# Performance work log

Measured on AMD Instinct MI355X. Metric: run time of the kernel, lower is better.

## Reference

```python
import jax, jax.numpy as jnp
import numpy as np
from jax import lax

CONF_THRESH = 0.5   # from module __init__
NMS_THRESH = 0.4    # from module __init__
TOP_K = 1000        # static pre-NMS candidate cap (JAX needs fixed shapes)

B, N, C = 16, 22743, 80  # batch, predictions (608px, 3 scales), COCO classes


def setup_inputs() -> dict:
    key = jax.random.key(0)
    # YOLOv3 raw output: [B, N, 5+C] = (cx, cy, w, h, obj, cls_0..cls_{C-1})
    v3_out = jax.random.uniform(key, (B, N, 5 + C), dtype=jnp.float32)
    return {"v3_out": v3_out}


def _xywh2xyxy(b):
    cx, cy, w, h = b[..., 0], b[..., 1], b[..., 2], b[..., 3]
    return jnp.stack([cx - w * 0.5, cy - h * 0.5, cx + w * 0.5, cy + h * 0.5], axis=-1)


def _pairwise_iou(boxes):
    # boxes: [K, 4] in xyxy -> [K, K] IoU
    x1 = jnp.maximum(boxes[:, None, 0], boxes[None, :, 0])
    y1 = jnp.maximum(boxes[:, None, 1], boxes[None, :, 1])
    x2 = jnp.minimum(boxes[:, None, 2], boxes[None, :, 2])
    y2 = jnp.minimum(boxes[:, None, 3], boxes[None, :, 3])
    inter = jnp.clip(x2 - x1, 0.0) * jnp.clip(y2 - y1, 0.0)
    area = jnp.clip(boxes[:, 2] - boxes[:, 0], 0.0) * jnp.clip(boxes[:, 3] - boxes[:, 1], 0.0)
    union = area[:, None] + area[None, :] - inter
    return inter / (union + 1e-16)


def _nms_image(pred):
    # pred: [N, 5+C]
    boxes = _xywh2xyxy(pred[:, :4])                 # [N, 4]
    obj = pred[:, 4]
    cls_conf = jnp.max(pred[:, 5:], axis=-1)        # best class confidence
    cls_id = jnp.argmax(pred[:, 5:], axis=-1)       # best class index
    # confidence filter (obj >= thresh) folded into the sort key
    score = jnp.where(obj >= CONF_THRESH, obj * cls_conf, -1.0)
    top_score, idx = lax.top_k(score, TOP_K)        # sorted descending by score
    valid = top_score > 0.0                          # survivors of the conf filter

    boxes_k = boxes[idx]          # [K, 4]
    obj_k = obj[idx]
    conf_k = cls_conf[idx]
    cls_k = cls_id[idx]

    iou = _pairwise_iou(boxes_k)                                   # [K, K]
    suppress = (iou > NMS_THRESH) & (cls_k[:, None] == cls_k[None, :])

    # greedy NMS over the score-sorted list: box i (if kept) kills later overlaps
    later = jnp.arange(TOP_K)

    def step(i, keep):
        kill = suppress[i] & (later > i) & keep[i]
        return keep & ~kill

    keep = lax.fori_loop(0, TOP_K, step, valid)

    # detections: (x1, y1, x2, y2, obj_conf, cls_conf, cls_id), zeroed where dropped
    dets = jnp.concatenate(
        [boxes_k, obj_k[:, None], conf_k[:, None], cls_k.astype(jnp.float32)[:, None]],
        axis=-1,
    )
    return dets * keep[:, None].astype(dets.dtype)   # [K, 7]


def reference(v3_out):
    # [B, K, 7] padded detections per image (zero rows = suppressed/invalid)
    return jax.vmap(_nms_image)(v3_out)
```

## Files before the change

kernel.cpp:

```cpp
#include <hip/hip_runtime.h>
#include <cstdint>

#pragma clang fp contract(off)

constexpr int cB = 16;
constexpr int cN = 22743;
constexpr int cROW = 85;
constexpr int cK = 1000;
constexpr float CONF_T = 0.5f;
constexpr float NMS_T = 0.4f;

__global__ __launch_bounds__(256) void k_score(const float* __restrict__ in,
                                               unsigned* __restrict__ ukey) {
  __shared__ float sdata[10880];
  constexpr int F4_PER_BLK = 2720;
  constexpr int TOTAL_F4 = (cB * cN * cROW) / 4;
  int tid = threadIdx.x;
  const float4* gin4 = (const float4*)in;
  float4* s4 = (float4*)sdata;
  int base_f4 = blockIdx.x * F4_PER_BLK;
#pragma unroll
  for (int q = 0; q < 11; ++q) {
    int k = tid + 256 * q;
    if (k < F4_PER_BLK) {
      int g = base_f4 + k;
      if (g < TOTAL_F4) s4[k] = gin4[g];
    }
  }
  __syncthreads();
  int r = tid >> 1, h = tid & 1;
  int grow = blockIdx.x * 128 + r;
  if (grow < cB * cN) {
    const float* rowp = sdata + cROW * r;
    int j0 = 5 + h * 40;
    float m0 = rowp[j0 + 0], m1 = rowp[j0 + 1];
    float m2 = rowp[j0 + 2], m3 = rowp[j0 + 3];
#pragma unroll
    for (int k = 4; k < 40; k += 4) {
      m0 = fmaxf(m0, rowp[j0 + k + 0]);
      m1 = fmaxf(m1, rowp[j0 + k + 1]);
      m2 = fmaxf(m2, rowp[j0 + k + 2]);
      m3 = fmaxf(m3, rowp[j0 + k + 3]);
    }
    float m = fmaxf(fmaxf(m0, m1), fmaxf(m2, m3));
    m = fmaxf(m, __shfl_xor(m, 1));
    if (h == 0) {
      float obj = rowp[4];
      unsigned u = 0u;
      if (obj >= CONF_T) {
        float s = obj * m;
        if (s > 0.0f) u = __float_as_uint(s);
      }
      ukey[grow] = u;
    }
  }
}

__device__ __forceinline__ void sort1024_u32_asc(unsigned* a, int tid) {
  for (int k = 2; k <= 1024; k <<= 1) {
    for (int j = k >> 1; j >= 1; j >>= 1) {
      __syncthreads();
      if (tid < 512) {
        int i = ((tid & ~(j - 1)) << 1) | (tid & (j - 1));
        int p = i | j;
        unsigned x = a[i], y = a[p];
        bool up = ((i & k) == 0);
        bool sw = up ? (x > y) : (x < y);
        if (sw) { a[i] = y; a[p] = x; }
      }
    }
  }
  __syncthreads();
}

__global__ __launch_bounds__(1024) void k_topk(const unsigned* __restrict__ ukey,
                                               int* __restrict__ topidx) {
  __shared__ unsigned hist[2048];
  __shared__ unsigned wtot[16];
  __shared__ unsigned long long cand[1024];
  __shared__ unsigned eqbuf[1024];
  __shared__ unsigned sh_T, sh_newrank, sh_E, sh_cnt;
  int img = blockIdx.x;
  int tid = threadIdx.x;
  int lane = tid & 63;
  int wv = tid >> 6;
  const unsigned* uk = ukey + (size_t)img * cN;

  unsigned prefix = 0;
  int bits = 0;
  unsigned rank = cK;
  unsigned gtc = 0;
  unsigned E = 0;

  for (int r = 0; r < 3; ++r) {
    int nb = (r < 2) ? 11 : 10;
    int shift = 32 - bits - nb;
    hist[tid] = 0u; hist[tid + 1024] = 0u;
    __syncthreads();
    for (int i0 = 0; i0 < cN; i0 += 1024) {
      int i = i0 + tid;
      unsigned u = (i < cN) ? uk[i] : 0u;
      bool inr = (i < cN);
      bool match = inr && (bits == 0 || (u >> (32 - bits)) == prefix);
      bool isz = match && (u == 0u);
      bool nz = match && (u != 0u);
      unsigned long long mz = __ballot(isz);
      if (isz && lane == (__ffsll((long long)mz) - 1))
        atomicAdd(&hist[0], (unsigned)__popcll(mz));
      if (nz) atomicAdd(&hist[(u >> shift) & ((1u << nb) - 1u)], 1u);
    }
    __syncthreads();
    unsigned h0 = hist[2 * tid];
    unsigned h1 = hist[2 * tid + 1];
    unsigned s2 = h0 + h1;
#pragma unroll
    for (int s = 1; s < 64; s <<= 1) {
      unsigned t = __shfl_down(s2, s);
      s2 += (lane + s < 64) ? t : 0u;
    }
    if (lane == 0) wtot[wv] = s2;
    __syncthreads();
    unsigned above = 0;
    for (int w2 = wv + 1; w2 < 16; ++w2) above += wtot[w2];
    unsigned S_even = above + s2;
    unsigned S_odd = S_even - h0;
    unsigned S_next = S_odd - h1;
    if (S_even >= rank && S_odd < rank) { sh_T = 2u * tid; sh_newrank = rank - S_odd; sh_E = h0; }
    if (S_odd >= rank && S_next < rank) { sh_T = 2u * tid + 1u; sh_newrank = rank - S_next; sh_E = h1; }
    __syncthreads();
    unsigned T = sh_T;
    unsigned nr = sh_newrank;
    E = sh_E;
    gtc += rank - nr;
    rank = nr;
    prefix = (prefix << nb) | T;
    bits += nb;
    __syncthreads();
    if (gtc + E <= 1024u) break;
  }

  bool tiepath = (gtc + E > 1024u);
  unsigned pivotLo = (bits >= 32) ? prefix : (prefix << (32 - bits));
  cand[tid] = (unsigned long long)tid;
  eqbuf[tid] = 0xFFFFFFFFu;
  if (tid == 0) sh_cnt = 0u;
  __syncthreads();

  if (!tiepath) {
    for (int i0 = 0; i0 < cN; i0 += 1024) {
      int i = i0 + tid;
      unsigned u = (i < cN) ? uk[i] : 0u;
      bool m = (i < cN) && (u >= pivotLo);
      unsigned long long mb = __ballot(m);
      if (m) {
        int ldr = __ffsll((long long)mb) - 1;
        unsigned base = 0;
        if (lane == ldr) base = atomicAdd(&sh_cnt, (unsigned)__popcll(mb));
        base = __shfl(base, ldr);
        unsigned pos = base + (unsigned)__popcll(mb & ((1ull << lane) - 1ull));
        if (pos < 1024u)
          cand[pos] = ((unsigned long long)u << 32) |
                      (unsigned long long)(0xFFFFFFFFu - (unsigned)i);
      }
    }
    __syncthreads();
  } else {
    unsigned P = prefix;
    for (int i0 = 0; i0 < cN; i0 += 1024) {
      int i = i0 + tid;
      unsigned u = (i < cN) ? uk[i] : 0u;
      bool gt = (i < cN) && (u > P);
      unsigned long long mb = __ballot(gt);
      if (gt) {
        int ldr = __ffsll((long long)mb) - 1;
        unsigned base = 0;
        if (lane == ldr) base = atomicAdd(&sh_cnt, (unsigned)__popcll(mb));
        base = __shfl(base, ldr);
        unsigned pos = base + (unsigned)__popcll(mb & ((1ull << lane) - 1ull));
        if (pos < 1024u)
          cand[pos] = ((unsigned long long)u << 32) |
                      (unsigned long long)(0xFFFFFFFFu - (unsigned)i);
      }
    }
    __syncthreads();
    if (tid == 0) sh_E = 0u;
    __syncthreads();
    for (int i0 = 0; i0 < cN; i0 += 1024) {
      int i = i0 + tid;
      unsigned u = (i < cN) ? uk[i] : 0u;
      bool eq = (i < cN) && (u == P);
      unsigned long long mb = __ballot(eq);
      if (eq) {
        int ldr = __ffsll((long long)mb) - 1;
        unsigned base = 0;
        if (lane == ldr) base = atomicAdd(&sh_E, (unsigned)__popcll(mb));
        base = __shfl(base, ldr);
        unsigned pos = base + (unsigned)__popcll(mb & ((1ull << lane) - 1ull));
        if (pos < 1024u) eqbuf[pos] = (unsigned)i;
      }
    }
    __syncthreads();
    sort1024_u32_asc(eqbuf, tid);
    int need = (int)cK - (int)gtc;
    for (int t = tid; t < need; t += 1024) {
      unsigned idx = eqbuf[t];
      if (idx != 0xFFFFFFFFu)
        cand[gtc + (unsigned)t] = ((unsigned long long)P << 32) |
                                  (unsigned long long)(0xFFFFFFFFu - idx);
    }
    __syncthreads();
  }

  unsigned long long my = cand[tid];
  unsigned rk = 0;
#pragma unroll 8
  for (int j = 0; j < 1024; ++j) rk += (cand[j] > my) ? 1u : 0u;
  if (rk < (unsigned)cK) {
    unsigned uhi = (unsigned)(my >> 32);
    int idx = (int)(0xFFFFFFFFu - (unsigned)(my & 0xFFFFFFFFull));
    topidx[img * cK + (int)rk] = (uhi > 0u) ? idx : -1;
  }
}

__global__ __launch_bounds__(256) void k_gather(const float* __restrict__ in,
                                                const int* __restrict__ topidx,
                                                float4* __restrict__ boxes,
                                                float* __restrict__ area,
                                                float* __restrict__ objv,
                                                float* __restrict__ confv,
                                                int* __restrict__ clsv,
                                                int* __restrict__ validv) {
  int wid = (int)((blockIdx.x * 256u + threadIdx.x) >> 6);
  int lane = threadIdx.x & 63;
  if (wid >= cB * cK) return;
  int img = wid / cK;
  int idx = topidx[wid];
  if (idx < 0) {
    if (lane == 0) {
      boxes[wid] = make_float4(0.f, 0.f, 0.f, 0.f);
      area[wid] = 0.f; objv[wid] = 0.f; confv[wid] = 0.f;
      clsv[wid] = -1; validv[wid] = 0;
    }
    return;
  }
  const float* row = in + ((size_t)img * cN + (size_t)idx) * cROW;
  float v = row[5 + lane];
  int ci = lane;
  if (lane < 16) {
    float v2 = row[69 + lane];
    if (v2 > v) { v = v2; ci = 64 + lane; }
  }
#pragma unroll
  for (int m = 1; m < 64; m <<= 1) {
    float ov = __shfl_xor(v, m);
    int oc = __shfl_xor(ci, m);
    if (ov > v || (ov == v && oc < ci)) { v = ov; ci = oc; }
  }
  if (lane == 0) {
    float cx = row[0], cy = row[1], w = row[2], h = row[3], ob = row[4];
    float hw = w * 0.5f, hh = h * 0.5f;
    float x1 = cx - hw, y1 = cy - hh, x2 = cx + hw, y2 = cy + hh;
    boxes[wid] = make_float4(x1, y1, x2, y2);
    area[wid] = fmaxf(x2 - x1, 0.f) * fmaxf(y2 - y1, 0.f);
    objv[wid] = ob; confv[wid] = v; clsv[wid] = ci; validv[wid] = 1;
  }
}

__global__ __launch_bounds__(256) void k_suppress(const float4* __restrict__ boxes,
                                                  const float* __restrict__ area,
                                                  const int* __restrict__ clsv,
                                                  unsigned* __restrict__ St) {
  __shared__ float sx1[1056], sy1[1056], sx2[1056], sy2[1056], sar[1056];
  __shared__ int scls[1056];
  int img = blockIdx.x >> 7;
  int rb = (blockIdx.x & 127) * 8;
  int tid = threadIdx.x;
  for (int i = tid; i < 1024; i += 256) {
    int p = i + (i >> 5);
    if (i < cK) {
      float4 b = boxes[img * cK + i];
      sx1[p] = b.x; sy1[p] = b.y; sx2[p] = b.z; sy2[p] = b.w;
      sar[p] = area[img * cK + i];
      scls[p] = clsv[img * cK + i];
    } else {
      sx1[p] = 0.f; sy1[p] = 0.f; sx2[p] = 0.f; sy2[p] = 0.f; sar[p] = 0.f;
      scls[p] = -2;
    }
  }
  __syncthreads();
  int i = rb + (tid >> 5);
  int w = tid & 31;
  int pi = i + (i >> 5);
  float bx1 = sx1[pi], by1 = sy1[pi], bx2 = sx2[pi], by2 = sy2[pi], ba = sar[pi];
  int bc = scls[pi];
  unsigned word = 0u;
#pragma unroll 4
  for (int bit = 0; bit < 32; ++bit) {
    int pj = 33 * w + bit;
    float xx1 = fmaxf(bx1, sx1[pj]);
    float yy1 = fmaxf(by1, sy1[pj]);
    float xx2 = fminf(bx2, sx2[pj]);
    float yy2 = fminf(by2, sy2[pj]);
    float inter = fmaxf(xx2 - xx1, 0.f) * fmaxf(yy2 - yy1, 0.f);
    float uni = ba + sar[pj] - inter;
    float iou = inter / (uni + 1e-16f);
    if (iou > NMS_T && bc == scls[pj]) word |= (1u << bit);
  }
  St[((size_t)(img * 32 + w)) * 1024 + (size_t)i] = word;
}

__device__ __forceinline__ unsigned u4c(const uint4& v, int c) {
  return c == 0 ? v.x : c == 1 ? v.y : c == 2 ? v.z : v.w;
}

__device__ __forceinline__ void nms_load(const uint4* __restrict__ colv, int b,
                                         uint4 (&buf)[8]) {
#pragma unroll
  for (int q = 0; q < 8; ++q) buf[q] = colv[8 * b + q];
}

__device__ __forceinline__ void nms_proc(int b, int lane, unsigned& kw,
                                         const uint4 (&W)[8]) {
  unsigned dec = 0u;
  if (lane == b) {
    unsigned kwb = kw;
#pragma unroll
    for (int t = 0; t < 32; ++t) {
      if ((kwb >> t) & 1u) {
        dec |= (1u << t);
        unsigned rw = u4c(W[t >> 2], t & 3);
        unsigned mgt = (t == 31) ? 0u : (0xFFFFFFFFu << (t + 1));
        kwb &= ~(rw & mgt);
      }
    }
    kw = kwb;
  }
  dec = __shfl(dec, b);
  if (lane > b) {
#pragma unroll
    for (int t = 0; t < 32; ++t) {
      unsigned sel = 0u - ((dec >> t) & 1u);
      kw &= ~(u4c(W[t >> 2], t & 3) & sel);
    }
  }
}

__global__ __launch_bounds__(64) void k_nms(const unsigned* __restrict__ St,
                                            const int* __restrict__ validv,
                                            const float4* __restrict__ boxes,
                                            const float* __restrict__ objv,
                                            const float* __restrict__ confv,
                                            const int* __restrict__ clsv,
                                            float* __restrict__ out) {
  __shared__ unsigned keep_sh[32];
  int img = blockIdx.x;
  int lane = threadIdx.x;
  if (lane < 32) {
    const uint4* colv = (const uint4*)(St + ((size_t)(img * 32 + lane)) * 1024);
    unsigned kw = 0u;
    for (int b = 0; b < 32; ++b) {
      int k = (lane << 5) + b;
      if (k < cK && validv[img * cK + k]) kw |= (1u << b);
    }
    uint4 bufA[8], bufB[8];
    nms_load(colv, 0, bufA);
    for (int b = 0; b < 32; b += 2) {
      if (b + 1 < 32) nms_load(colv, b + 1, bufB);
      nms_proc(b, lane, kw, bufA);
      if (b + 2 < 32) nms_load(colv, b + 2, bufA);
      nms_proc(b + 1, lane, kw, bufB);
    }
    keep_sh[lane] = kw;
  }
  __syncthreads();
  for (int k = lane; k < cK; k += 64) {
    bool kp = ((keep_sh[k >> 5] >> (k & 31)) & 1u) != 0u;
    size_t o = ((size_t)img * cK + (size_t)k) * 7;
    if (kp) {
      float4 b = boxes[img * cK + k];
      out[o + 0] = b.x; out[o + 1] = b.y; out[o + 2] = b.z; out[o + 3] = b.w;
      out[o + 4] = objv[img * cK + k];
      out[o + 5] = confv[img * cK + k];
      out[o + 6] = (float)clsv[img * cK + k];
    } else {
      out[o + 0] = 0.f; out[o + 1] = 0.f; out[o + 2] = 0.f; out[o + 3] = 0.f;
      out[o + 4] = 0.f; out[o + 5] = 0.f; out[o + 6] = 0.f;
    }
  }
}

extern "C" void kernel_launch(void* const* d_in, const int* in_sizes, int n_in,
                              void* d_out, int out_size, void* d_ws, size_t ws_size,
                              hipStream_t stream) {
  const float* in = (const float*)d_in[0];
  float* out = (float*)d_out;
  char* ws = (char*)d_ws;
  size_t off = 0;
  auto take = [&](size_t bytes) {
    size_t r = off;
    off += (bytes + 255) & ~(size_t)255;
    return r;
  };
  unsigned* ukey = (unsigned*)(ws + take((size_t)cB * cN * 4));
  int* topidx = (int*)(ws + take((size_t)cB * cK * 4));
  float4* boxes = (float4*)(ws + take((size_t)cB * cK * 16));
  float* area = (float*)(ws + take((size_t)cB * cK * 4));
  float* objv = (float*)(ws + take((size_t)cB * cK * 4));
  float* confv = (float*)(ws + take((size_t)cB * cK * 4));
  int* clsv = (int*)(ws + take((size_t)cB * cK * 4));
  int* validv = (int*)(ws + take((size_t)cB * cK * 4));
  unsigned* St = (unsigned*)(ws + take((size_t)cB * 32 * 1024 * 4));

  int nrows = cB * cN;
  int blocks1 = (nrows + 127) / 128;
  k_score<<<blocks1, 256, 0, stream>>>(in, ukey);
  k_topk<<<cB, 1024, 0, stream>>>(ukey, topidx);
  int waves3 = cB * cK;
  k_gather<<<(waves3 * 64 + 255) / 256, 256, 0, stream>>>(in, topidx, boxes, area,
                                                          objv, confv, clsv, validv);
  k_suppress<<<cB * 128, 256, 0, stream>>>(boxes, area, clsv, St);
  k_nms<<<cB, 64, 0, stream>>>(St, validv, boxes, objv, confv, clsv, out);
}
```

Baseline: 281.8 us.

## Cache top-k keys in registers and restructure suppress-mask build with ballots

The top-k kernel now loads each image's keys into per-thread registers once, instead of re-reading global memory in every radix pass and in every compaction pass. The suppress kernel switches to packed float4/float2 shared-memory layouts where each lane tests a strided column, and it assembles the 32-bit mask words with wave ballots instead of a per-thread serial bit loop. The register array adds pressure at 1024 threads per block, and the ballot-based word assembly depends on the 64-lane wave split into 32-lane halves.

```diff
diff --git a/kernel.cpp b/kernel.cpp
--- a/kernel.cpp
+++ b/kernel.cpp
@@ -72,6 +72,8 @@
   }
   __syncthreads();
 }
+
+constexpr int TK_IT = (cN + 1023) / 1024;
 
 __global__ __launch_bounds__(1024) void k_topk(const unsigned* __restrict__ ukey,
                                                int* __restrict__ topidx) {
@@ -86,6 +88,13 @@
   int wv = tid >> 6;
   const unsigned* uk = ukey + (size_t)img * cN;
 
+  unsigned uv[TK_IT];
+#pragma unroll
+  for (int q = 0; q < TK_IT; ++q) {
+    int i = q * 1024 + tid;
+    uv[q] = (i < cN) ? uk[i] : 0u;
+  }
+
   unsigned prefix = 0;
   int bits = 0;
   unsigned rank = cK;
@@ -95,19 +104,20 @@
   for (int r = 0; r < 3; ++r) {
     int nb = (r < 2) ? 11 : 10;
     int shift = 32 - bits - nb;
+    unsigned bmask = (1u << nb) - 1u;
     hist[tid] = 0u; hist[tid + 1024] = 0u;
     __syncthreads();
-    for (int i0 = 0; i0 < cN; i0 += 1024) {
-      int i = i0 + tid;
-      unsigned u = (i < cN) ? uk[i] : 0u;
-      bool inr = (i < cN);
-      bool match = inr && (bits == 0 || (u >> (32 - bits)) == prefix);
+#pragma unroll
+    for (int q = 0; q < TK_IT; ++q) {
+      int i = q * 1024 + tid;
+      unsigned u = uv[q];
+      bool match = (i < cN) && (bits == 0 || (u >> (32 - bits)) == prefix);
       bool isz = match && (u == 0u);
       bool nz = match && (u != 0u);
       unsigned long long mz = __ballot(isz);
       if (isz && lane == (__ffsll((long long)mz) - 1))
         atomicAdd(&hist[0], (unsigned)__popcll(mz));
-      if (nz) atomicAdd(&hist[(u >> shift) & ((1u << nb) - 1u)], 1u);
+      if (nz) atomicAdd(&hist[(u >> shift) & bmask], 1u);
     }
     __syncthreads();
     unsigned h0 = hist[2 * tid];
@@ -147,9 +157,10 @@
   __syncthreads();
 
   if (!tiepath) {
-    for (int i0 = 0; i0 < cN; i0 += 1024) {
-      int i = i0 + tid;
-      unsigned u = (i < cN) ? uk[i] : 0u;
+#pragma unroll
+    for (int q = 0; q < TK_IT; ++q) {
+      int i = q * 1024 + tid;
+      unsigned u = uv[q];
       bool m = (i < cN) && (u >= pivotLo);
       unsigned long long mb = __ballot(m);
       if (m) {
@@ -166,9 +177,9 @@
     __syncthreads();
   } else {
     unsigned P = prefix;
-    for (int i0 = 0; i0 < cN; i0 += 1024) {
-      int i = i0 + tid;
-      unsigned u = (i < cN) ? uk[i] : 0u;
+    for (int q = 0; q < TK_IT; ++q) {
+      int i = q * 1024 + tid;
+      unsigned u = uv[q];
       bool gt = (i < cN) && (u > P);
       unsigned long long mb = __ballot(gt);
       if (gt) {
@@ -185,9 +196,9 @@
     __syncthreads();
     if (tid == 0) sh_E = 0u;
     __syncthreads();
-    for (int i0 = 0; i0 < cN; i0 += 1024) {
-      int i = i0 + tid;
-      unsigned u = (i < cN) ? uk[i] : 0u;
+    for (int q = 0; q < TK_IT; ++q) {
+      int i = q * 1024 + tid;
+      unsigned u = uv[q];
       bool eq = (i < cN) && (u == P);
       unsigned long long mb = __ballot(eq);
       if (eq) {
@@ -270,41 +281,47 @@
                                                   const float* __restrict__ area,
                                                   const int* __restrict__ clsv,
                                                   unsigned* __restrict__ St) {
-  __shared__ float sx1[1056], sy1[1056], sx2[1056], sy2[1056], sar[1056];
-  __shared__ int scls[1056];
+  __shared__ float4 sbox[1024];
+  __shared__ float2 sac[1024];
   int img = blockIdx.x >> 7;
   int rb = (blockIdx.x & 127) * 8;
   int tid = threadIdx.x;
   for (int i = tid; i < 1024; i += 256) {
-    int p = i + (i >> 5);
     if (i < cK) {
-      float4 b = boxes[img * cK + i];
-      sx1[p] = b.x; sy1[p] = b.y; sx2[p] = b.z; sy2[p] = b.w;
-      sar[p] = area[img * cK + i];
-      scls[p] = clsv[img * cK + i];
+      sbox[i] = boxes[img * cK + i];
+      float2 t;
+      t.x = area[img * cK + i];
+      t.y = __int_as_float(clsv[img * cK + i]);
+      sac[i] = t;
     } else {
-      sx1[p] = 0.f; sy1[p] = 0.f; sx2[p] = 0.f; sy2[p] = 0.f; sar[p] = 0.f;
-      scls[p] = -2;
+      sbox[i] = make_float4(0.f, 0.f, 0.f, 0.f);
+      float2 t; t.x = 0.f; t.y = __int_as_float(-2);
+      sac[i] = t;
     }
   }
   __syncthreads();
   int i = rb + (tid >> 5);
   int w = tid & 31;
-  int pi = i + (i >> 5);
-  float bx1 = sx1[pi], by1 = sy1[pi], bx2 = sx2[pi], by2 = sy2[pi], ba = sar[pi];
-  int bc = scls[pi];
+  float4 bb = sbox[i];
+  float2 bac = sac[i];
+  float ba = bac.x;
+  int bc = __float_as_int(bac.y);
   unsigned word = 0u;
-#pragma unroll 4
-  for (int bit = 0; bit < 32; ++bit) {
-    int pj = 33 * w + bit;
-    float xx1 = fmaxf(bx1, sx1[pj]);
-    float yy1 = fmaxf(by1, sy1[pj]);
-    float xx2 = fminf(bx2, sx2[pj]);
-    float yy2 = fminf(by2, sy2[pj]);
+#pragma unroll 8
+  for (int blk = 0; blk < 32; ++blk) {
+    int j = (blk << 5) | w;
+    float4 jb = sbox[j];
+    float2 ja = sac[j];
+    float xx1 = fmaxf(bb.x, jb.x);
+    float yy1 = fmaxf(bb.y, jb.y);
+    float xx2 = fminf(bb.z, jb.z);
+    float yy2 = fminf(bb.w, jb.w);
     float inter = fmaxf(xx2 - xx1, 0.f) * fmaxf(yy2 - yy1, 0.f);
-    float uni = ba + sar[pj] - inter;
+    float uni = ba + ja.x - inter;
     float iou = inter / (uni + 1e-16f);
-    if (iou > NMS_T && bc == scls[pj]) word |= (1u << bit);
+    bool sup = (iou > NMS_T) && (bc == __float_as_int(ja.y));
+    unsigned long long mk = __ballot(sup);
+    if (blk == w) word = (tid & 32) ? (unsigned)(mk >> 32) : (unsigned)mk;
   }
   St[((size_t)(img * 32 + w)) * 1024 + (size_t)i] = word;
 }
```

Measured after the change: 282.9 us. Within noise of the previous version (+0.4%).
